# Kernel optimization log

Hardware: AMD Instinct MI355X
Metric: run time of the kernel (lower is better)

The kernel has to match this reference:

```python
import jax, jax.numpy as jnp
import numpy as np

D_MODEL = 1024
NUM_HEADS = 16
NEG_INF = jnp.float32(-(2.0 ** 32) + 1.0)  # matches TF's -2**32+1 padding value


def setup_inputs() -> dict:
    key = jax.random.key(0)
    ks = jax.random.split(key, 10)
    B, S, D = 4, 1024, D_MODEL
    s = 1.0 / np.sqrt(D)
    return {
        "q": jax.random.normal(ks[0], (B, S, D), jnp.float32),
        "k": jax.random.normal(ks[1], (B, S, D), jnp.float32),
        "v": jax.random.normal(ks[2], (B, S, D), jnp.float32),
        "mask": jax.random.randint(ks[3], (NUM_HEADS * B, 1, S), 0, 2, jnp.int32),
        "Wq": jax.random.normal(ks[4], (D, D), jnp.float32) * s,
        "bq": jnp.zeros((D,), jnp.float32),
        "Wk": jax.random.normal(ks[5], (D, D), jnp.float32) * s,
        "bk": jnp.zeros((D,), jnp.float32),
        "Wv": jax.random.normal(ks[6], (D, D), jnp.float32) * s,
        "bv": jnp.zeros((D,), jnp.float32),
    }


def _split_heads(x, h):
    # TF: concat(split(x, h, axis=2), axis=0) -> head index leading on batch dim
    B, S, D = x.shape
    dh = D // h
    return x.reshape(B, S, h, dh).transpose(2, 0, 1, 3).reshape(h * B, S, dh)


def _merge_heads(x, h):
    hB, S, dh = x.shape
    B = hB // h
    return x.reshape(h, B, S, dh).transpose(1, 2, 0, 3).reshape(B, S, h * dh)


def reference(q, k, v, mask, Wq, bq, Wk, bk, Wv, bv):
    h = NUM_HEADS
    qp = q @ Wq + bq
    kp = k @ Wk + bk
    vp = v @ Wv + bv
    qh = _split_heads(qp, h)  # [h*B, S, dh]
    kh = _split_heads(kp, h)
    vh = _split_heads(vp, h)
    dh = kh.shape[-1]
    logits = jnp.einsum('bqd,bkd->bqk', qh, kh) / jnp.sqrt(jnp.float32(dh))
    logits = jnp.where(mask == 0, NEG_INF, logits)  # padding mask, broadcast [h*B,1,S]
    S = qh.shape[1]
    causal = jnp.tril(jnp.ones((S, S), jnp.bool_))
    logits = jnp.where(causal[None], logits, NEG_INF)
    attn = jax.nn.softmax(logits, axis=-1)
    out = jnp.einsum('bqk,bkd->bqd', attn, vh)
    return _merge_heads(out, h)  # [B, S, d_model]
```

## Files before the change

### kernel.cpp

```cpp
#include <hip/hip_runtime.h>
#include <stdint.h>

#define DEV __device__ __forceinline__

typedef __attribute__((ext_vector_type(4))) float f32x4;
typedef __attribute__((ext_vector_type(8))) __bf16 bf16x8;
typedef __attribute__((ext_vector_type(8))) unsigned short ushort8;

DEV unsigned short f2bf(float f) {
    union { float f; unsigned int u; } v; v.f = f;
    unsigned int r = v.u + 0x7FFFu + ((v.u >> 16) & 1u);
    return (unsigned short)(r >> 16);
}
DEV float bf2f(unsigned short u) {
    union { unsigned int u; float f; } v; v.u = ((unsigned int)u) << 16;
    return v.f;
}
DEV int swz(int o) { return o ^ ((o >> 3) & 0x70); }

DEV void gload_lds16(const void* gptr, void* lptr) {
    __builtin_amdgcn_global_load_lds(
        (const __attribute__((address_space(1))) unsigned int*)gptr,
        (__attribute__((address_space(3))) unsigned int*)lptr, 16, 0, 0);
}

__global__ void k_convert(const float* __restrict__ q, const float* __restrict__ k,
                          const float* __restrict__ v, unsigned short* __restrict__ qb,
                          unsigned short* __restrict__ kb, unsigned short* __restrict__ vb) {
    const int z = blockIdx.z;
    const float* src = z == 0 ? q : (z == 1 ? k : v);
    unsigned short* dst = z == 0 ? qb : (z == 1 ? kb : vb);
    const size_t idx = ((size_t)blockIdx.x * 256 + threadIdx.x) * 8;
    f32x4 a = *(const f32x4*)(src + idx);
    f32x4 b = *(const f32x4*)(src + idx + 4);
    ushort8 o;
    o[0] = f2bf(a[0]); o[1] = f2bf(a[1]); o[2] = f2bf(a[2]); o[3] = f2bf(a[3]);
    o[4] = f2bf(b[0]); o[5] = f2bf(b[1]); o[6] = f2bf(b[2]); o[7] = f2bf(b[3]);
    *(ushort8*)(dst + idx) = o;
}

__global__ void k_convw(const float* __restrict__ Wq, const float* __restrict__ Wk,
                        const float* __restrict__ Wv, unsigned short* __restrict__ wt) {
    __shared__ float tile[64 * 65];
    const int z = blockIdx.z;
    const float* W = z == 0 ? Wq : (z == 1 ? Wk : Wv);
    unsigned short* dst = wt + (size_t)z * 1048576;
    const int k0 = blockIdx.x * 64, n0 = blockIdx.y * 64;
    const int t = threadIdx.x;
#pragma unroll
    for (int i = 0; i < 4; i++) {
        const int idx = i * 256 + t;
        const int row = idx >> 4, c4 = (idx & 15) * 4;
        f32x4 val = *(const f32x4*)(W + (size_t)(k0 + row) * 1024 + n0 + c4);
#pragma unroll
        for (int j = 0; j < 4; j++) tile[row * 65 + c4 + j] = val[j];
    }
    __syncthreads();
#pragma unroll
    for (int i = 0; i < 2; i++) {
        const int idx = i * 256 + t;
        const int nrow = idx >> 3, c8 = (idx & 7) * 8;
        ushort8 o;
#pragma unroll
        for (int j = 0; j < 8; j++) o[j] = f2bf(tile[(c8 + j) * 65 + nrow]);
        *(ushort8*)(dst + (size_t)(n0 + nrow) * 1024 + k0 + c8) = o;
    }
}

__global__ __launch_bounds__(256) void k_proj(
    const unsigned short* __restrict__ qb, const unsigned short* __restrict__ kb,
    const unsigned short* __restrict__ vb, const unsigned short* __restrict__ wt,
    const float* __restrict__ bq, const float* __restrict__ bk, const float* __restrict__ bv,
    unsigned short* __restrict__ qh, unsigned short* __restrict__ kh,
    unsigned short* __restrict__ vh) {
    const int z = blockIdx.z;
    const unsigned short* A  = z == 0 ? qb : (z == 1 ? kb : vb);
    const unsigned short* Bt = wt + (size_t)z * 1048576;
    const float* bias = z == 0 ? bq : (z == 1 ? bk : bv);
    unsigned short* outp = z == 0 ? qh : (z == 1 ? kh : vh);
    const float scale = z == 0 ? 0.18033688011112042f : 1.0f;

    __shared__ unsigned short sA[128 * 64];
    __shared__ unsigned short sB[128 * 64];

    const int tid = threadIdx.x;
    const int w = tid >> 6, lane = tid & 63;
    const int c = lane & 15, gq = lane >> 4;
    const int wrow = w >> 1, wcol = w & 1;
    const int m0 = blockIdx.y * 128, n0 = blockIdx.x * 128;
    const int lr = lane >> 3;
    const int lcs = ((lane & 7) ^ (lane >> 3)) * 8;

    f32x4 acc[4][4] = {};

    for (int kt = 0; kt < 16; kt++) {
        __syncthreads();
        const int kb0 = kt * 64;
#pragma unroll
        for (int i = 0; i < 4; i++) {
            const int rbase = w * 32 + i * 8;
            gload_lds16(A  + (size_t)(m0 + rbase + lr) * 1024 + kb0 + lcs,
                        (char*)sA + rbase * 128);
            gload_lds16(Bt + (size_t)(n0 + rbase + lr) * 1024 + kb0 + lcs,
                        (char*)sB + rbase * 128);
        }
        __syncthreads();
#pragma unroll
        for (int kk = 0; kk < 2; kk++) {
            bf16x8 af[4], bfr[4];
#pragma unroll
            for (int i = 0; i < 4; i++) {
                af[i]  = *(const bf16x8*)((char*)sA +
                          swz((wrow * 64 + i * 16 + c) * 128 + kk * 64 + gq * 16));
                bfr[i] = *(const bf16x8*)((char*)sB +
                          swz((wcol * 64 + i * 16 + c) * 128 + kk * 64 + gq * 16));
            }
#pragma unroll
            for (int mi = 0; mi < 4; mi++)
#pragma unroll
                for (int ni = 0; ni < 4; ni++)
                    acc[mi][ni] = __builtin_amdgcn_mfma_f32_16x16x32_bf16(
                        af[mi], bfr[ni], acc[mi][ni], 0, 0, 0);
        }
    }

    float bvals[4];
#pragma unroll
    for (int ni = 0; ni < 4; ni++) bvals[ni] = bias[n0 + wcol * 64 + ni * 16 + c];

#pragma unroll
    for (int mi = 0; mi < 4; mi++)
#pragma unroll
        for (int ni = 0; ni < 4; ni++) {
            const int n = n0 + wcol * 64 + ni * 16 + c;
            const int head = n >> 6, d = n & 63;
#pragma unroll
            for (int r = 0; r < 4; r++) {
                const int m = m0 + wrow * 64 + mi * 16 + gq * 4 + r;
                const int bb = m >> 10, s = m & 1023;
                const float val = (acc[mi][ni][r] + bvals[ni]) * scale;
                outp[(size_t)((head << 2) + bb) * 65536 + (size_t)s * 64 + d] = f2bf(val);
            }
        }
}

__global__ void k_trv(const unsigned short* __restrict__ vh, unsigned short* __restrict__ vt,
                      float* __restrict__ vmean) {
    __shared__ unsigned int tile[64 * 65];
    const int hb = blockIdx.y, s0 = blockIdx.x * 64;
    const int t = threadIdx.x;
#pragma unroll
    for (int it = 0; it < 2; it++) {
        const int idx = it * 256 + t;
        const int row = idx >> 3, c8 = (idx & 7) * 8;
        ushort8 val = *(const ushort8*)(vh + (size_t)hb * 65536 + (size_t)(s0 + row) * 64 + c8);
#pragma unroll
        for (int j = 0; j < 8; j++) tile[row * 65 + c8 + j] = val[j];
    }
    __syncthreads();
#pragma unroll
    for (int it = 0; it < 2; it++) {
        const int idx = it * 256 + t;
        const int d = idx >> 3, s8 = (idx & 7) * 8;
        ushort8 o;
#pragma unroll
        for (int j = 0; j < 8; j++) o[j] = (unsigned short)tile[(s8 + j) * 65 + d];
        *(ushort8*)(vt + (size_t)hb * 65536 + (size_t)d * 1024 + s0 + s8) = o;
    }
    if (t < 64) {
        float sum = 0.f;
        for (int s = 0; s < 64; s++) sum += bf2f((unsigned short)tile[s * 65 + t]);
        atomicAdd(&vmean[hb * 64 + t], sum * (1.0f / 1024.0f));
    }
}

__global__ __launch_bounds__(256) void k_attn(
    const unsigned short* __restrict__ qh, const unsigned short* __restrict__ kh,
    const unsigned short* __restrict__ vt, const int* __restrict__ mask,
    const float* __restrict__ vmean, float* __restrict__ out,
    char* __restrict__ part) {
    __shared__ unsigned short sK[2][64 * 64];
    __shared__ unsigned short sV[2][64 * 64];
    __shared__ unsigned short sP[4 * 16 * 64];

    const int idx = blockIdx.x, hb = blockIdx.y;
    int qt, ch, nch;
    if (idx < 4)       { qt = idx;                 ch = 0;             nch = 1; }
    else if (idx < 12) { qt = 4 + ((idx - 4) >> 1);  ch = (idx - 4) & 1;  nch = 2; }
    else if (idx < 24) { int r = idx - 12; qt = 8 + r / 3; ch = r % 3;   nch = 3; }
    else               { qt = 12 + ((idx - 24) >> 2); ch = (idx - 24) & 3; nch = 4; }
    const int t0 = ch * 4;
    const int t1 = min(t0 + 4, qt + 1);

    const int tid = threadIdx.x;
    const int w = tid >> 6, lane = tid & 63;
    const int c = lane & 15, g = lane >> 4;
    const int q0 = qt * 64 + w * 16;
    const size_t hboff = (size_t)hb * 65536;
    const int* mp = mask + hb * 1024;

    bf16x8 aq[2];
#pragma unroll
    for (int kk = 0; kk < 2; kk++)
        aq[kk] = *(const bf16x8*)(qh + hboff + (size_t)(q0 + c) * 64 + kk * 32 + g * 8);

    f32x4 oacc[4] = {};
    float lsum[4] = {0.f, 0.f, 0.f, 0.f};
    float mrow[4] = {-1e30f, -1e30f, -1e30f, -1e30f};
    unsigned short* pw = sP + w * 1024;

    const int srow = tid >> 3, sch = tid & 7;
    const int ssc = (sch ^ (srow & 7)) * 8;

    auto stage = [&](int t, int buf) {
        const int kv0 = t * 64;
#pragma unroll
        for (int i = 0; i < 2; i++) {
            const int row = i * 32 + srow;
            gload_lds16(kh + hboff + (size_t)(kv0 + row) * 64 + ssc,
                        (char*)sK[buf] + row * 128 + sch * 16);
        }
#pragma unroll
        for (int i = 0; i < 2; i++) {
            const int row = i * 32 + srow;
            gload_lds16(vt + hboff + (size_t)row * 1024 + kv0 + ssc,
                        (char*)sV[buf] + row * 128 + sch * 16);
        }
    };

    stage(t0, 0);
    for (int t = t0; t < t1; t++) {
        const int cur = (t - t0) & 1;
        if (t + 1 < t1) {
            stage(t + 1, cur ^ 1);
            asm volatile("s_waitcnt vmcnt(4)" ::: "memory");
        } else {
            asm volatile("s_waitcnt vmcnt(0)" ::: "memory");
        }
        __builtin_amdgcn_s_barrier();
        __builtin_amdgcn_sched_barrier(0);

        const int kv0 = t * 64;
        const bool diag = (t == qt);
        const unsigned short* sKc = sK[cur];
        const unsigned short* sVc = sV[cur];

        f32x4 sacc[4] = {};
#pragma unroll
        for (int ns = 0; ns < 4; ns++) {
            const int kvl = ns * 16 + c;
#pragma unroll
            for (int kk = 0; kk < 2; kk++) {
                bf16x8 bk = *(const bf16x8*)((char*)sKc + swz(kvl * 128 + kk * 64 + g * 16));
                sacc[ns] = __builtin_amdgcn_mfma_f32_16x16x32_bf16(aq[kk], bk, sacc[ns], 0, 0, 0);
            }
        }
        float sv[4][4];
#pragma unroll
        for (int ns = 0; ns < 4; ns++) {
            const int kvg = kv0 + ns * 16 + c;
            const int mv = mp[kvg];
#pragma unroll
            for (int r = 0; r < 4; r++) {
                const bool ok = (mv != 0) && (!diag || kvg <= q0 + g * 4 + r);
                sv[ns][r] = ok ? sacc[ns][r] : -1e30f;
            }
        }
#pragma unroll
        for (int r = 0; r < 4; r++) {
            float vmax = fmaxf(fmaxf(sv[0][r], sv[1][r]), fmaxf(sv[2][r], sv[3][r]));
            vmax = fmaxf(vmax, __shfl_xor(vmax, 1, 64));
            vmax = fmaxf(vmax, __shfl_xor(vmax, 2, 64));
            vmax = fmaxf(vmax, __shfl_xor(vmax, 4, 64));
            vmax = fmaxf(vmax, __shfl_xor(vmax, 8, 64));
            const float mnew = fmaxf(mrow[r], vmax);
            const float alpha = exp2f(mrow[r] - mnew);
            mrow[r] = mnew;
            float rs = 0.f;
            const int ql = g * 4 + r;
#pragma unroll
            for (int ns = 0; ns < 4; ns++) {
                const float pv = exp2f(sv[ns][r] - mnew);
                rs += pv;
                *(unsigned short*)((char*)pw + swz(ql * 128 + (ns * 16 + c) * 2)) = f2bf(pv);
            }
            rs += __shfl_xor(rs, 1, 64);
            rs += __shfl_xor(rs, 2, 64);
            rs += __shfl_xor(rs, 4, 64);
            rs += __shfl_xor(rs, 8, 64);
            lsum[r] = lsum[r] * alpha + rs;
#pragma unroll
            for (int nd = 0; nd < 4; nd++) oacc[nd][r] *= alpha;
        }
        asm volatile("s_waitcnt lgkmcnt(0)" ::: "memory");
#pragma unroll
        for (int ks = 0; ks < 2; ks++) {
            const bf16x8 ap = *(const bf16x8*)((char*)pw + swz(c * 128 + ks * 64 + g * 16));
#pragma unroll
            for (int nd = 0; nd < 4; nd++) {
                const int d = nd * 16 + c;
                const bf16x8 bvv = *(const bf16x8*)((char*)sVc + swz(d * 128 + ks * 64 + g * 16));
                oacc[nd] = __builtin_amdgcn_mfma_f32_16x16x32_bf16(ap, bvv, oacc[nd], 0, 0, 0);
            }
        }
        __builtin_amdgcn_sched_barrier(0);
        __builtin_amdgcn_s_barrier();
        __builtin_amdgcn_sched_barrier(0);
    }

    if (nch == 1) {
        const int bidx = hb & 3, head = hb >> 2;
#pragma unroll
        for (int nd = 0; nd < 4; nd++)
#pragma unroll
            for (int r = 0; r < 4; r++) {
                const int s = q0 + g * 4 + r;
                const int dcol = nd * 16 + c;
                const float val = (mrow[r] < -5e29f) ? vmean[hb * 64 + dcol]
                                                     : oacc[nd][r] / lsum[r];
                out[(size_t)bidx * 1048576 + (size_t)s * 1024 + head * 64 + dcol] = val;
            }
    } else {
        char* sp = part + ((size_t)hb * 36 + (idx - 4)) * 8704;
        unsigned short* op = (unsigned short*)sp;
#pragma unroll
        for (int nd = 0; nd < 4; nd++)
#pragma unroll
            for (int r = 0; r < 4; r++)
                op[(w * 16 + g * 4 + r) * 64 + nd * 16 + c] = f2bf(oacc[nd][r]);
        if (c == 0) {
            float* mo = (float*)(sp + 8192);
            float* lo = (float*)(sp + 8448);
#pragma unroll
            for (int r = 0; r < 4; r++) {
                mo[w * 16 + g * 4 + r] = mrow[r];
                lo[w * 16 + g * 4 + r] = lsum[r];
            }
        }
    }
}

__global__ __launch_bounds__(256) void k_combine(
    const char* __restrict__ part, const float* __restrict__ vmean,
    float* __restrict__ out) {
    const int qt = 4 + blockIdx.x, hb = blockIdx.y;
    int nch, base;
    if (qt < 8)       { nch = 2; base = (qt - 4) * 2; }
    else if (qt < 12) { nch = 3; base = 8 + (qt - 8) * 3; }
    else              { nch = 4; base = 20 + (qt - 12) * 4; }
    const int t = threadIdx.x;
    const int row = t >> 2, d0 = (t & 3) * 16;
    const char* sp0 = part + ((size_t)hb * 36 + base) * 8704;

    float mi[4], li[4];
    float m = -1e30f;
#pragma unroll
    for (int i = 0; i < 4; i++)
        if (i < nch) {
            const char* sp = sp0 + (size_t)i * 8704;
            mi[i] = ((const float*)(sp + 8192))[row];
            li[i] = ((const float*)(sp + 8448))[row];
            m = fmaxf(m, mi[i]);
        }
    float L = 0.f;
    float o[16];
#pragma unroll
    for (int j = 0; j < 16; j++) o[j] = 0.f;
#pragma unroll
    for (int i = 0; i < 4; i++)
        if (i < nch) {
            const float wgt = exp2f(mi[i] - m);
            L += wgt * li[i];
            const unsigned short* op =
                (const unsigned short*)(sp0 + (size_t)i * 8704) + row * 64 + d0;
            ushort8 a = *(const ushort8*)op;
            ushort8 b = *(const ushort8*)(op + 8);
#pragma unroll
            for (int j = 0; j < 8; j++) {
                o[j]     += wgt * bf2f(a[j]);
                o[8 + j] += wgt * bf2f(b[j]);
            }
        }
    const int bidx = hb & 3, head = hb >> 2;
    float* dst = out + (size_t)bidx * 1048576 + (size_t)(qt * 64 + row) * 1024 + head * 64 + d0;
    if (L > 0.f) {
        const float inv = 1.0f / L;
#pragma unroll
        for (int j = 0; j < 16; j++) dst[j] = o[j] * inv;
    } else {
#pragma unroll
        for (int j = 0; j < 16; j++) dst[j] = vmean[hb * 64 + d0 + j];
    }
}

extern "C" void kernel_launch(void* const* d_in, const int* in_sizes, int n_in,
                              void* d_out, int out_size, void* d_ws, size_t ws_size,
                              hipStream_t stream) {
    const float* q  = (const float*)d_in[0];
    const float* k  = (const float*)d_in[1];
    const float* v  = (const float*)d_in[2];
    const int* mask = (const int*)d_in[3];
    const float* Wq = (const float*)d_in[4];
    const float* bq = (const float*)d_in[5];
    const float* Wk = (const float*)d_in[6];
    const float* bk = (const float*)d_in[7];
    const float* Wv = (const float*)d_in[8];
    const float* bv = (const float*)d_in[9];
    float* out = (float*)d_out;

    unsigned short* qb = (unsigned short*)d_ws;
    unsigned short* kb = qb + 4194304;
    unsigned short* vb = kb + 4194304;
    unsigned short* wt = vb + 4194304;
    unsigned short* qh = wt + 3 * 1048576;
    unsigned short* kh = qh + 4194304;
    unsigned short* vh = kh + 4194304;
    unsigned short* vt = vh + 4194304;
    float* vmean = (float*)(vt + 4194304);
    char* part = (char*)qb;

    k_convert<<<dim3(2048, 1, 3), 256, 0, stream>>>(q, k, v, qb, kb, vb);
    k_convw<<<dim3(16, 16, 3), 256, 0, stream>>>(Wq, Wk, Wv, wt);
    k_proj<<<dim3(8, 32, 3), 256, 0, stream>>>(qb, kb, vb, wt, bq, bk, bv, qh, kh, vh);
    hipMemsetAsync(vmean, 0, 64 * 64 * sizeof(float), stream);
    k_trv<<<dim3(16, 64), 256, 0, stream>>>(vh, vt, vmean);
    k_attn<<<dim3(40, 64), 256, 0, stream>>>(qh, kh, vt, mask, vmean, out, part);
    k_combine<<<dim3(12, 64), 256, 0, stream>>>(part, vmean, out);
}
```

Measured before the change: 222.1 us.

## Write V transposed from projection, drop LDS staging in attention, transpose S layout

The projection epilogue for V now writes the transposed layout directly, which removes the separate transpose kernel, the memset and the atomics. The mean of V is computed by a small dedicated kernel instead. The attention kernel stops staging K/V through double-buffered LDS and reads MFMA operands straight from global memory, removing block barriers. It also computes S^T so each lane owns one query row, which cuts shuffle reductions and lets packed bf16 conversion write P. The cost is uncached, less coalesced global reads of K and V in the inner loop.

```diff
diff --git a/kernel.cpp b/kernel.cpp
--- a/kernel.cpp
+++ b/kernel.cpp
@@ -6,6 +6,9 @@
 typedef __attribute__((ext_vector_type(4))) float f32x4;
 typedef __attribute__((ext_vector_type(8))) __bf16 bf16x8;
 typedef __attribute__((ext_vector_type(8))) unsigned short ushort8;
+typedef __attribute__((ext_vector_type(4))) unsigned short u16x4;
+typedef __attribute__((ext_vector_type(4))) int i32x4;
+typedef __attribute__((ext_vector_type(2))) unsigned int u32x2;
 
 DEV unsigned short f2bf(float f) {
     union { float f; unsigned int u; } v; v.f = f;
@@ -15,6 +18,11 @@
 DEV float bf2f(unsigned short u) {
     union { unsigned int u; float f; } v; v.u = ((unsigned int)u) << 16;
     return v.f;
+}
+DEV unsigned int cvt_pk_bf16(float lo, float hi) {
+    unsigned int r;
+    asm("v_cvt_pk_bf16_f32 %0, %1, %2" : "=v"(r) : "v"(lo), "v"(hi));
+    return r;
 }
 DEV int swz(int o) { return o ^ ((o >> 3) & 0x70); }
 
@@ -72,12 +80,11 @@
     const unsigned short* __restrict__ vb, const unsigned short* __restrict__ wt,
     const float* __restrict__ bq, const float* __restrict__ bk, const float* __restrict__ bv,
     unsigned short* __restrict__ qh, unsigned short* __restrict__ kh,
-    unsigned short* __restrict__ vh) {
+    unsigned short* __restrict__ vt) {
     const int z = blockIdx.z;
     const unsigned short* A  = z == 0 ? qb : (z == 1 ? kb : vb);
     const unsigned short* Bt = wt + (size_t)z * 1048576;
     const float* bias = z == 0 ? bq : (z == 1 ? bk : bv);
-    unsigned short* outp = z == 0 ? qh : (z == 1 ? kh : vh);
     const float scale = z == 0 ? 0.18033688011112042f : 1.0f;
 
     __shared__ unsigned short sA[128 * 64];
@@ -128,50 +135,56 @@
 #pragma unroll
     for (int ni = 0; ni < 4; ni++) bvals[ni] = bias[n0 + wcol * 64 + ni * 16 + c];
 
-#pragma unroll
-    for (int mi = 0; mi < 4; mi++)
-#pragma unroll
-        for (int ni = 0; ni < 4; ni++) {
-            const int n = n0 + wcol * 64 + ni * 16 + c;
-            const int head = n >> 6, d = n & 63;
-#pragma unroll
-            for (int r = 0; r < 4; r++) {
-                const int m = m0 + wrow * 64 + mi * 16 + gq * 4 + r;
-                const int bb = m >> 10, s = m & 1023;
-                const float val = (acc[mi][ni][r] + bvals[ni]) * scale;
-                outp[(size_t)((head << 2) + bb) * 65536 + (size_t)s * 64 + d] = f2bf(val);
-            }
-        }
-}
-
-__global__ void k_trv(const unsigned short* __restrict__ vh, unsigned short* __restrict__ vt,
-                      float* __restrict__ vmean) {
-    __shared__ unsigned int tile[64 * 65];
-    const int hb = blockIdx.y, s0 = blockIdx.x * 64;
-    const int t = threadIdx.x;
-#pragma unroll
-    for (int it = 0; it < 2; it++) {
-        const int idx = it * 256 + t;
-        const int row = idx >> 3, c8 = (idx & 7) * 8;
-        ushort8 val = *(const ushort8*)(vh + (size_t)hb * 65536 + (size_t)(s0 + row) * 64 + c8);
-#pragma unroll
-        for (int j = 0; j < 8; j++) tile[row * 65 + c8 + j] = val[j];
-    }
+    if (z < 2) {
+        unsigned short* outp = z == 0 ? qh : kh;
+#pragma unroll
+        for (int mi = 0; mi < 4; mi++)
+#pragma unroll
+            for (int ni = 0; ni < 4; ni++) {
+                const int n = n0 + wcol * 64 + ni * 16 + c;
+                const int head = n >> 6, d = n & 63;
+#pragma unroll
+                for (int r = 0; r < 4; r++) {
+                    const int m = m0 + wrow * 64 + mi * 16 + gq * 4 + r;
+                    const int bb = m >> 10, s = m & 1023;
+                    const float val = (acc[mi][ni][r] + bvals[ni]) * scale;
+                    outp[(size_t)((head << 2) + bb) * 65536 + (size_t)s * 64 + d] = f2bf(val);
+                }
+            }
+    } else {
+#pragma unroll
+        for (int mi = 0; mi < 4; mi++)
+#pragma unroll
+            for (int ni = 0; ni < 4; ni++) {
+                const int n = n0 + wcol * 64 + ni * 16 + c;
+                const int head = n >> 6, d = n & 63;
+                const int mbase = m0 + wrow * 64 + mi * 16 + gq * 4;
+                const int bb = mbase >> 10, sloc = mbase & 1023;
+                u16x4 o;
+#pragma unroll
+                for (int r = 0; r < 4; r++) o[r] = f2bf(acc[mi][ni][r] + bvals[ni]);
+                *(u16x4*)(vt + (size_t)((head << 2) + bb) * 65536 +
+                          (size_t)d * 1024 + sloc) = o;
+            }
+    }
+}
+
+__global__ void k_vmean(const unsigned short* __restrict__ vt, float* __restrict__ vmean) {
+    __shared__ float red[256];
+    const int hb = blockIdx.x, t = threadIdx.x;
+    const int d = t >> 2, part = t & 3;
+    const unsigned short* p = vt + (size_t)hb * 65536 + (size_t)d * 1024 + part * 256;
+    float sum = 0.f;
+#pragma unroll 4
+    for (int i = 0; i < 32; i++) {
+        ushort8 v8 = *(const ushort8*)(p + i * 8);
+#pragma unroll
+        for (int j = 0; j < 8; j++) sum += bf2f(v8[j]);
+    }
+    red[t] = sum;
     __syncthreads();
-#pragma unroll
-    for (int it = 0; it < 2; it++) {
-        const int idx = it * 256 + t;
-        const int d = idx >> 3, s8 = (idx & 7) * 8;
-        ushort8 o;
-#pragma unroll
-        for (int j = 0; j < 8; j++) o[j] = (unsigned short)tile[(s8 + j) * 65 + d];
-        *(ushort8*)(vt + (size_t)hb * 65536 + (size_t)d * 1024 + s0 + s8) = o;
-    }
-    if (t < 64) {
-        float sum = 0.f;
-        for (int s = 0; s < 64; s++) sum += bf2f((unsigned short)tile[s * 65 + t]);
-        atomicAdd(&vmean[hb * 64 + t], sum * (1.0f / 1024.0f));
-    }
+    if (part == 0)
+        vmean[hb * 64 + d] = (red[t] + red[t + 1] + red[t + 2] + red[t + 3]) * (1.0f / 1024.0f);
 }
 
 __global__ __launch_bounds__(256) void k_attn(
@@ -179,8 +192,6 @@
     const unsigned short* __restrict__ vt, const int* __restrict__ mask,
     const float* __restrict__ vmean, float* __restrict__ out,
     char* __restrict__ part) {
-    __shared__ unsigned short sK[2][64 * 64];
-    __shared__ unsigned short sV[2][64 * 64];
     __shared__ unsigned short sP[4 * 16 * 64];
 
     const int idx = blockIdx.x, hb = blockIdx.y;
@@ -194,130 +205,113 @@
 
     const int tid = threadIdx.x;
     const int w = tid >> 6, lane = tid & 63;
-    const int c = lane & 15, g = lane >> 4;
+    const int c = lane & 15, g = lane >> 4, g4 = g * 4;
     const int q0 = qt * 64 + w * 16;
+    const int qg = q0 + c;
     const size_t hboff = (size_t)hb * 65536;
     const int* mp = mask + hb * 1024;
+    unsigned short* pw = sP + w * 1024;
 
     bf16x8 aq[2];
 #pragma unroll
     for (int kk = 0; kk < 2; kk++)
-        aq[kk] = *(const bf16x8*)(qh + hboff + (size_t)(q0 + c) * 64 + kk * 32 + g * 8);
+        aq[kk] = *(const bf16x8*)(qh + hboff + (size_t)qg * 64 + kk * 32 + g * 8);
 
     f32x4 oacc[4] = {};
-    float lsum[4] = {0.f, 0.f, 0.f, 0.f};
-    float mrow[4] = {-1e30f, -1e30f, -1e30f, -1e30f};
-    unsigned short* pw = sP + w * 1024;
-
-    const int srow = tid >> 3, sch = tid & 7;
-    const int ssc = (sch ^ (srow & 7)) * 8;
-
-    auto stage = [&](int t, int buf) {
-        const int kv0 = t * 64;
-#pragma unroll
-        for (int i = 0; i < 2; i++) {
-            const int row = i * 32 + srow;
-            gload_lds16(kh + hboff + (size_t)(kv0 + row) * 64 + ssc,
-                        (char*)sK[buf] + row * 128 + sch * 16);
-        }
-#pragma unroll
-        for (int i = 0; i < 2; i++) {
-            const int row = i * 32 + srow;
-            gload_lds16(vt + hboff + (size_t)row * 1024 + kv0 + ssc,
-                        (char*)sV[buf] + row * 128 + sch * 16);
-        }
-    };
-
-    stage(t0, 0);
+    float lsum = 0.f, mrow = -1e30f;
+
     for (int t = t0; t < t1; t++) {
-        const int cur = (t - t0) & 1;
-        if (t + 1 < t1) {
-            stage(t + 1, cur ^ 1);
-            asm volatile("s_waitcnt vmcnt(4)" ::: "memory");
-        } else {
-            asm volatile("s_waitcnt vmcnt(0)" ::: "memory");
-        }
-        __builtin_amdgcn_s_barrier();
-        __builtin_amdgcn_sched_barrier(0);
-
         const int kv0 = t * 64;
         const bool diag = (t == qt);
-        const unsigned short* sKc = sK[cur];
-        const unsigned short* sVc = sV[cur];
+        const unsigned short* Kt = kh + hboff + (size_t)kv0 * 64;
+        const unsigned short* Vt = vt + hboff + kv0;
 
         f32x4 sacc[4] = {};
 #pragma unroll
+        for (int ns = 0; ns < 4; ns++)
+#pragma unroll
+            for (int kk = 0; kk < 2; kk++) {
+                const bf16x8 bk = *(const bf16x8*)(Kt + (size_t)(ns * 16 + c) * 64 +
+                                                   kk * 32 + g * 8);
+                sacc[ns] = __builtin_amdgcn_mfma_f32_16x16x32_bf16(bk, aq[kk], sacc[ns], 0, 0, 0);
+            }
+
+        float sv[4][4];
+        float mx = -1e30f;
+#pragma unroll
         for (int ns = 0; ns < 4; ns++) {
-            const int kvl = ns * 16 + c;
-#pragma unroll
-            for (int kk = 0; kk < 2; kk++) {
-                bf16x8 bk = *(const bf16x8*)((char*)sKc + swz(kvl * 128 + kk * 64 + g * 16));
-                sacc[ns] = __builtin_amdgcn_mfma_f32_16x16x32_bf16(aq[kk], bk, sacc[ns], 0, 0, 0);
-            }
-        }
-        float sv[4][4];
+            const i32x4 mm = *(const i32x4*)(mp + kv0 + ns * 16 + g4);
+#pragma unroll
+            for (int r = 0; r < 4; r++) {
+                float s = (mm[r] != 0) ? sacc[ns][r] : -1e30f;
+                if (diag) s = (kv0 + ns * 16 + g4 + r <= qg) ? s : -1e30f;
+                sv[ns][r] = s;
+                mx = fmaxf(mx, s);
+            }
+        }
+        mx = fmaxf(mx, __shfl_xor(mx, 16, 64));
+        mx = fmaxf(mx, __shfl_xor(mx, 32, 64));
+        const float mnew = fmaxf(mrow, mx);
+        const float alpha = exp2f(mrow - mnew);
+        mrow = mnew;
+
+        float rs = 0.f;
+        u32x2 pk[4];
 #pragma unroll
         for (int ns = 0; ns < 4; ns++) {
-            const int kvg = kv0 + ns * 16 + c;
-            const int mv = mp[kvg];
-#pragma unroll
-            for (int r = 0; r < 4; r++) {
-                const bool ok = (mv != 0) && (!diag || kvg <= q0 + g * 4 + r);
-                sv[ns][r] = ok ? sacc[ns][r] : -1e30f;
-            }
-        }
-#pragma unroll
-        for (int r = 0; r < 4; r++) {
-            float vmax = fmaxf(fmaxf(sv[0][r], sv[1][r]), fmaxf(sv[2][r], sv[3][r]));
-            vmax = fmaxf(vmax, __shfl_xor(vmax, 1, 64));
-            vmax = fmaxf(vmax, __shfl_xor(vmax, 2, 64));
-            vmax = fmaxf(vmax, __shfl_xor(vmax, 4, 64));
-            vmax = fmaxf(vmax, __shfl_xor(vmax, 8, 64));
-            const float mnew = fmaxf(mrow[r], vmax);
-            const float alpha = exp2f(mrow[r] - mnew);
-            mrow[r] = mnew;
-            float rs = 0.f;
-            const int ql = g * 4 + r;
-#pragma unroll
-            for (int ns = 0; ns < 4; ns++) {
-                const float pv = exp2f(sv[ns][r] - mnew);
-                rs += pv;
-                *(unsigned short*)((char*)pw + swz(ql * 128 + (ns * 16 + c) * 2)) = f2bf(pv);
-            }
-            rs += __shfl_xor(rs, 1, 64);
-            rs += __shfl_xor(rs, 2, 64);
-            rs += __shfl_xor(rs, 4, 64);
-            rs += __shfl_xor(rs, 8, 64);
-            lsum[r] = lsum[r] * alpha + rs;
-#pragma unroll
-            for (int nd = 0; nd < 4; nd++) oacc[nd][r] *= alpha;
-        }
+            const float e0 = exp2f(sv[ns][0] - mnew);
+            const float e1 = exp2f(sv[ns][1] - mnew);
+            const float e2 = exp2f(sv[ns][2] - mnew);
+            const float e3 = exp2f(sv[ns][3] - mnew);
+            rs += (e0 + e1) + (e2 + e3);
+            pk[ns][0] = cvt_pk_bf16(e0, e1);
+            pk[ns][1] = cvt_pk_bf16(e2, e3);
+        }
+        rs += __shfl_xor(rs, 16, 64);
+        rs += __shfl_xor(rs, 32, 64);
+        lsum = lsum * alpha + rs;
+
+#pragma unroll
+        for (int ns = 0; ns < 4; ns++)
+            *(u32x2*)((char*)pw + swz(c * 128 + (ns * 16 + g4) * 2)) = pk[ns];
+
+        float av[4];
+#pragma unroll
+        for (int r = 0; r < 4; r++) av[r] = __shfl(alpha, g4 + r, 16);
+#pragma unroll
+        for (int nd = 0; nd < 4; nd++)
+#pragma unroll
+            for (int r = 0; r < 4; r++) oacc[nd][r] *= av[r];
+
         asm volatile("s_waitcnt lgkmcnt(0)" ::: "memory");
 #pragma unroll
         for (int ks = 0; ks < 2; ks++) {
             const bf16x8 ap = *(const bf16x8*)((char*)pw + swz(c * 128 + ks * 64 + g * 16));
 #pragma unroll
             for (int nd = 0; nd < 4; nd++) {
-                const int d = nd * 16 + c;
-                const bf16x8 bvv = *(const bf16x8*)((char*)sVc + swz(d * 128 + ks * 64 + g * 16));
+                const bf16x8 bvv = *(const bf16x8*)(Vt + (size_t)(nd * 16 + c) * 1024 +
+                                                    ks * 32 + g * 8);
                 oacc[nd] = __builtin_amdgcn_mfma_f32_16x16x32_bf16(ap, bvv, oacc[nd], 0, 0, 0);
             }
         }
-        __builtin_amdgcn_sched_barrier(0);
-        __builtin_amdgcn_s_barrier();
-        __builtin_amdgcn_sched_barrier(0);
     }
 
     if (nch == 1) {
         const int bidx = hb & 3, head = hb >> 2;
+        float lf[4], mf[4];
+#pragma unroll
+        for (int r = 0; r < 4; r++) {
+            lf[r] = __shfl(lsum, g4 + r, 16);
+            mf[r] = __shfl(mrow, g4 + r, 16);
+        }
 #pragma unroll
         for (int nd = 0; nd < 4; nd++)
 #pragma unroll
             for (int r = 0; r < 4; r++) {
-                const int s = q0 + g * 4 + r;
+                const int s = q0 + g4 + r;
                 const int dcol = nd * 16 + c;
-                const float val = (mrow[r] < -5e29f) ? vmean[hb * 64 + dcol]
-                                                     : oacc[nd][r] / lsum[r];
+                const float val = (mf[r] < -5e29f) ? vmean[hb * 64 + dcol]
+                                                   : oacc[nd][r] / lf[r];
                 out[(size_t)bidx * 1048576 + (size_t)s * 1024 + head * 64 + dcol] = val;
             }
     } else {
@@ -327,15 +321,12 @@
         for (int nd = 0; nd < 4; nd++)
 #pragma unroll
             for (int r = 0; r < 4; r++)
-                op[(w * 16 + g * 4 + r) * 64 + nd * 16 + c] = f2bf(oacc[nd][r]);
-        if (c == 0) {
+                op[(w * 16 + g4 + r) * 64 + nd * 16 + c] = f2bf(oacc[nd][r]);
+        if (g == 0) {
             float* mo = (float*)(sp + 8192);
             float* lo = (float*)(sp + 8448);
-#pragma unroll
-            for (int r = 0; r < 4; r++) {
-                mo[w * 16 + g * 4 + r] = mrow[r];
-                lo[w * 16 + g * 4 + r] = lsum[r];
-            }
+            mo[w * 16 + c] = mrow;
+            lo[w * 16 + c] = lsum;
         }
     }
 }
@@ -383,7 +374,7 @@
         }
     const int bidx = hb & 3, head = hb >> 2;
     float* dst = out + (size_t)bidx * 1048576 + (size_t)(qt * 64 + row) * 1024 + head * 64 + d0;
-    if (L > 0.f) {
+    if (m > -5e29f) {
         const float inv = 1.0f / L;
 #pragma unroll
         for (int j = 0; j < 16; j++) dst[j] = o[j] * inv;
@@ -421,9 +412,8 @@
 
     k_convert<<<dim3(2048, 1, 3), 256, 0, stream>>>(q, k, v, qb, kb, vb);
     k_convw<<<dim3(16, 16, 3), 256, 0, stream>>>(Wq, Wk, Wv, wt);
-    k_proj<<<dim3(8, 32, 3), 256, 0, stream>>>(qb, kb, vb, wt, bq, bk, bv, qh, kh, vh);
-    hipMemsetAsync(vmean, 0, 64 * 64 * sizeof(float), stream);
-    k_trv<<<dim3(16, 64), 256, 0, stream>>>(vh, vt, vmean);
+    k_proj<<<dim3(8, 32, 3), 256, 0, stream>>>(qb, kb, vb, wt, bq, bk, bv, qh, kh, vt);
+    k_vmean<<<64, 256, 0, stream>>>(vt, vmean);
     k_attn<<<dim3(40, 64), 256, 0, stream>>>(qh, kh, vt, mask, vmean, out, part);
     k_combine<<<dim3(12, 64), 256, 0, stream>>>(part, vmean, out);
 }
```

New measurement: 262.2 us. 1.18x slower.
